# Optimization experiments

Measured on AMD Instinct MI355X. Metric: run time of the kernel, lower is better.

## Reference

```python
import jax, jax.numpy as jnp
import numpy as np

N_NODES = 50000
N_EDGES = 800000
FEAT = 10
HID = 64
N_SHEETS = 256
SHEET_LEN = 128
NUM_GRAPHS = 1


def _glorot(key, shape):
    fan_in, fan_out = shape[0], shape[1]
    lim = float(np.sqrt(6.0 / (fan_in + fan_out)))
    return jax.random.uniform(key, shape, jnp.float32, -lim, lim)


def setup_inputs() -> dict:
    key = jax.random.key(0)
    ks = jax.random.split(key, 16)
    x = jax.random.normal(ks[0], (N_NODES, FEAT), jnp.float32)
    edge_index = jax.random.randint(ks[1], (2, N_EDGES), 0, N_NODES, jnp.int64)
    batch = jnp.zeros((N_NODES,), jnp.int64)
    sheet_node_idx = jax.random.randint(ks[2], (N_SHEETS, SHEET_LEN), 0, N_NODES, jnp.int64)
    sheet_features = jax.random.normal(ks[3], (N_SHEETS, FEAT), jnp.float32)
    return {
        "x": x, "edge_index": edge_index, "batch": batch,
        "sheet_node_idx": sheet_node_idx, "sheet_features": sheet_features,
        "W_gcn1": _glorot(ks[4], (FEAT, HID)), "b_gcn1": jnp.zeros((HID,), jnp.float32),
        "W_gcn2": _glorot(ks[5], (HID, HID)), "b_gcn2": jnp.zeros((HID,), jnp.float32),
        "W_gcn3": _glorot(ks[6], (HID, HID)), "b_gcn3": jnp.zeros((HID,), jnp.float32),
        "geo_W1": _glorot(ks[7], (FEAT, HID)), "geo_b1": jnp.zeros((HID,), jnp.float32),
        "geo_W2": _glorot(ks[8], (HID, HID)), "geo_b2": jnp.zeros((HID,), jnp.float32),
        "fus_W": _glorot(ks[9], (2 * HID, HID)), "fus_b": jnp.zeros((HID,), jnp.float32),
        "q_W1": _glorot(ks[10], (2 * HID, HID)), "q_b1": jnp.zeros((HID,), jnp.float32),
        "q_W2": _glorot(ks[11], (HID, 1)), "q_b2": jnp.zeros((1,), jnp.float32),
    }


def gcn_conv(x, W, b, src, dst, norm_edge, norm_self):
    # PyG GCNConv: h = x @ W, symmetric-normalized aggregation with self loops, + b
    h = x @ W                                  # [N, H]
    msg = h[src] * norm_edge[:, None]          # [E, H] gather
    agg = jax.ops.segment_sum(msg, dst, num_segments=x.shape[0])  # scatter-add
    agg = agg + h * norm_self[:, None]         # self-loop contribution
    return agg + b


def reference(x, edge_index, batch, sheet_node_idx, sheet_features,
              W_gcn1, b_gcn1, W_gcn2, b_gcn2, W_gcn3, b_gcn3,
              geo_W1, geo_b1, geo_W2, geo_b2, fus_W, fus_b,
              q_W1, q_b1, q_W2, q_b2):
    src, dst = edge_index[0], edge_index[1]
    N = x.shape[0]
    # degree with self loops (edge weights = 1), counted on destination
    deg = jax.ops.segment_sum(jnp.ones_like(dst, jnp.float32), dst, num_segments=N) + 1.0
    dinv = jax.lax.rsqrt(deg)
    norm_edge = dinv[src] * dinv[dst]   # [E]
    norm_self = dinv * dinv             # [N]

    h = jax.nn.relu(gcn_conv(x, W_gcn1, b_gcn1, src, dst, norm_edge, norm_self))
    h = jax.nn.relu(gcn_conv(h, W_gcn2, b_gcn2, src, dst, norm_edge, norm_self))
    h = jax.nn.relu(gcn_conv(h, W_gcn3, b_gcn3, src, dst, norm_edge, norm_self))

    # global mean pool over batch ids (single graph here)
    sums = jax.ops.segment_sum(h, batch, num_segments=NUM_GRAPHS)
    counts = jax.ops.segment_sum(jnp.ones((N,), jnp.float32), batch, num_segments=NUM_GRAPHS)
    g_emb = sums / counts[:, None]      # [1, H]

    # per-sheet mean pooling (equal-length sheets)
    sheet_embs = h[sheet_node_idx].mean(axis=1)            # [S, H]

    geo = jax.nn.relu(sheet_features @ geo_W1 + geo_b1) @ geo_W2 + geo_b2
    fused = jax.nn.relu(jnp.concatenate([sheet_embs, geo], axis=1) @ fus_W + fus_b)

    global_embs = jnp.broadcast_to(g_emb, (fused.shape[0], g_emb.shape[1]))
    hq = jnp.concatenate([fused, global_embs], axis=1)
    q = jax.nn.relu(hq @ q_W1 + q_b1) @ q_W2 + q_b2
    return q[:, 0]
```

## Files before the change

### kernel.cpp

```cpp
#include <hip/hip_runtime.h>

#define HID 64
#define FEAT 10
#define MAXSEG 8192

typedef unsigned short u16;

__device__ inline u16 f2bf(float f) {
    unsigned u = __float_as_uint(f);
    unsigned r = (u + 0x7fffu + ((u >> 16) & 1u)) >> 16;
    return (u16)r;
}
__device__ inline void bf8_add(float* acc, uint4 u) {
    acc[0] += __uint_as_float(u.x << 16);
    acc[1] += __uint_as_float(u.x & 0xffff0000u);
    acc[2] += __uint_as_float(u.y << 16);
    acc[3] += __uint_as_float(u.y & 0xffff0000u);
    acc[4] += __uint_as_float(u.z << 16);
    acc[5] += __uint_as_float(u.z & 0xffff0000u);
    acc[6] += __uint_as_float(u.w << 16);
    acc[7] += __uint_as_float(u.w & 0xffff0000u);
}


__global__ void histA(const int* __restrict__ dst, int* __restrict__ cnt2T,
                      int E, int nbuckets, int nchunks) {
    __shared__ int lh[256];
    int t = threadIdx.x, c = blockIdx.x;
    if (t < 256) lh[t] = 0;
    __syncthreads();
    int base = c * 4096;
    #pragma unroll
    for (int j = 0; j < 4; j++) {
        int e = base + t + j * 1024;
        if (e < E) atomicAdd(&lh[dst[e] >> 8], 1);
    }
    __syncthreads();
    if (t < nbuckets) cnt2T[t * nchunks + c] = lh[t];
}

__global__ void off2_local(const int* __restrict__ cnt2T, int* __restrict__ off2L,
                           int* __restrict__ tot, int nchunks) {
    __shared__ int lds[256];
    int b = blockIdx.x, t = threadIdx.x;
    int v = (t < nchunks) ? cnt2T[b * nchunks + t] : 0;
    lds[t] = v;
    __syncthreads();
    for (int off = 1; off < 256; off <<= 1) {
        int a = lds[t];
        int s = (t >= off) ? lds[t - off] : 0;
        __syncthreads();
        lds[t] = a + s;
        __syncthreads();
    }
    if (t < nchunks) off2L[b * nchunks + t] = lds[t] - v;
    if (t == 255) tot[b] = lds[255];
}

__global__ void base_scan(const int* __restrict__ tot, int* __restrict__ base, int nbuckets) {
    __shared__ int lds[256];
    int t = threadIdx.x;
    int v = (t < nbuckets) ? tot[t] : 0;
    lds[t] = v;
    __syncthreads();
    for (int off = 1; off < 256; off <<= 1) {
        int a = lds[t];
        int s = (t >= off) ? lds[t - off] : 0;
        __syncthreads();
        lds[t] = a + s;
        __syncthreads();
    }
    if (t < nbuckets) base[t] = lds[t] - v;
}

__global__ void binpass(const int* __restrict__ src, const int* __restrict__ dst,
                        const int* __restrict__ base, const int* __restrict__ off2L,
                        unsigned* __restrict__ tmp, int E, int nbuckets, int nchunks) {
    __shared__ int cur[256];
    int t = threadIdx.x, c = blockIdx.x;
    if (t < 256) cur[t] = (t < nbuckets) ? base[t] + off2L[t * nchunks + c] : 0;
    __syncthreads();
    int b0 = c * 4096;
    #pragma unroll
    for (int j = 0; j < 4; j++) {
        int e = b0 + t + j * 1024;
        if (e < E) {
            int s = src[e], d = dst[e];
            int slot = atomicAdd(&cur[d >> 8], 1);
            tmp[slot] = ((unsigned)(d & 255) << 16) | (unsigned)s;
        }
    }
}

__global__ void csr_build(const unsigned* __restrict__ tmp, const int* __restrict__ base,
                          const int* __restrict__ tot, u16* __restrict__ csr2,
                          int* __restrict__ row_start, int* __restrict__ row_cntp,
                          float* __restrict__ dinv, int N) {
    __shared__ __align__(16) u16 staged[MAXSEG];
    __shared__ int cntL[256], padL[256], scanL[256], curL[256];
    int b = blockIdx.x, t = threadIdx.x;
    if (t < 256) cntL[t] = 0;
    for (int i = t; i < MAXSEG; i += 1024) staged[i] = (u16)N;
    __syncthreads();
    int segBase = base[b], segLen = tot[b];
    for (int i = t; i < segLen; i += 1024)
        atomicAdd(&cntL[tmp[segBase + i] >> 16], 1);
    __syncthreads();
    if (t < 256) { padL[t] = (cntL[t] + 7) & ~7; scanL[t] = padL[t]; }
    __syncthreads();
    for (int off = 1; off < 256; off <<= 1) {
        int a = (t < 256) ? scanL[t] : 0;
        int s = (t >= off && t < 256) ? scanL[t - off] : 0;
        __syncthreads();
        if (t < 256) scanL[t] = a + s;
        __syncthreads();
    }
    if (t < 256) {
        int excl = scanL[t] - padL[t];
        curL[t] = excl;
        int node = b * 256 + t;
        if (node < N) {
            row_start[node] = b * MAXSEG + excl;
            row_cntp[node]  = padL[t];
            dinv[node]      = rsqrtf((float)cntL[t] + 1.0f);
        }
    }
    __syncthreads();
    for (int i = t; i < segLen; i += 1024) {
        unsigned e = tmp[segBase + i];
        int idx = atomicAdd(&curL[e >> 16], 1);
        staged[idx] = (u16)(e & 0xffffu);
    }
    __syncthreads();
    ((uint4*)(csr2 + (size_t)b * MAXSEG))[t] = ((const uint4*)staged)[t];
}

__global__ void zero_sentinel(u16* __restrict__ hwb, u16* __restrict__ xp, int N) {
    int t = threadIdx.x;
    if (t < 64) hwb[((size_t)(t >> 4) * (N + 1) + N) * 16 + (t & 15)] = 0;
    else if (t < 80) xp[(size_t)N * 16 + (t - 64)] = 0;
}


__global__ void pad_x(const float* __restrict__ x, const float* __restrict__ dinv,
                      u16* __restrict__ xp, int N) {
    int idx = blockIdx.x * 256 + threadIdx.x;
    if (idx >= N * 16) return;
    int n = idx >> 4, c = idx & 15;
    xp[idx] = (c < FEAT) ? f2bf(dinv[n] * x[n * FEAT + c]) : (u16)0;
}

__global__ void gather_x(const int* __restrict__ row_start, const int* __restrict__ row_cntp,
                         const u16* __restrict__ csr2, const u16* __restrict__ xp,
                         const float* __restrict__ dinv, float* __restrict__ aggx, int N) {
    int t = threadIdx.x;
    int node = blockIdx.x * 128 + (t >> 1);
    if (node >= N) return;
    int c0 = (t & 1) * 8;
    float acc[8] = {0.f,0.f,0.f,0.f,0.f,0.f,0.f,0.f};
    uint4 sv = *(const uint4*)(xp + (size_t)node * 16 + c0);
    bf8_add(acc, sv);
    int i0 = row_start[node], iE = i0 + row_cntp[node];
    for (int i = i0; i < iE; i += 8) {
        uint4 ev = *(const uint4*)(csr2 + i);
        int s0 = ev.x & 0xffff, s1 = ev.x >> 16;
        int s2 = ev.y & 0xffff, s3 = ev.y >> 16;
        int s4 = ev.z & 0xffff, s5 = ev.z >> 16;
        int s6 = ev.w & 0xffff, s7 = ev.w >> 16;
        uint4 u0 = *(const uint4*)(xp + (size_t)s0 * 16 + c0);
        uint4 u1 = *(const uint4*)(xp + (size_t)s1 * 16 + c0);
        uint4 u2 = *(const uint4*)(xp + (size_t)s2 * 16 + c0);
        uint4 u3 = *(const uint4*)(xp + (size_t)s3 * 16 + c0);
        uint4 u4 = *(const uint4*)(xp + (size_t)s4 * 16 + c0);
        uint4 u5 = *(const uint4*)(xp + (size_t)s5 * 16 + c0);
        uint4 u6 = *(const uint4*)(xp + (size_t)s6 * 16 + c0);
        uint4 u7 = *(const uint4*)(xp + (size_t)s7 * 16 + c0);
        bf8_add(acc, u0); bf8_add(acc, u1); bf8_add(acc, u2); bf8_add(acc, u3);
        bf8_add(acc, u4); bf8_add(acc, u5); bf8_add(acc, u6); bf8_add(acc, u7);
    }
    float di = dinv[node];
    float4 o0 = make_float4(acc[0]*di, acc[1]*di, acc[2]*di, acc[3]*di);
    float4 o1 = make_float4(acc[4]*di, acc[5]*di, acc[6]*di, acc[7]*di);
    *(float4*)(aggx + (size_t)node * 16 + c0)     = o0;
    *(float4*)(aggx + (size_t)node * 16 + c0 + 4) = o1;
}

__global__ void gcn_matmul1(const float* __restrict__ aggx, const float* __restrict__ W1,
                            const float* __restrict__ b1, float* __restrict__ h1, int N) {
    __shared__ float sW[FEAT * 64];
    __shared__ float sH[64 * 16];
    int t = threadIdx.x;
    int node0 = blockIdx.x * 64;
    for (int i = t; i < FEAT * 64; i += 256) sW[i] = W1[i];
    for (int i = t; i < 64 * 16; i += 256) {
        int r = i >> 4, k = i & 15;
        int node = node0 + r;
        sH[i] = (node < N) ? aggx[(size_t)node * 16 + k] : 0.0f;
    }
    __syncthreads();
    int c0 = (t & 15) * 4;
    int rbase = (t >> 4) * 4;
    float4 a0 = {0,0,0,0}, a1 = {0,0,0,0}, a2 = {0,0,0,0}, a3 = {0,0,0,0};
    for (int k = 0; k < FEAT; k++) {
        float4 w = *(const float4*)(sW + k * 64 + c0);
        float h0 = sH[(rbase + 0) * 16 + k];
        float h1v = sH[(rbase + 1) * 16 + k];
        float h2 = sH[(rbase + 2) * 16 + k];
        float h3 = sH[(rbase + 3) * 16 + k];
        a0.x += h0 * w.x; a0.y += h0 * w.y; a0.z += h0 * w.z; a0.w += h0 * w.w;
        a1.x += h1v * w.x; a1.y += h1v * w.y; a1.z += h1v * w.z; a1.w += h1v * w.w;
        a2.x += h2 * w.x; a2.y += h2 * w.y; a2.z += h2 * w.z; a2.w += h2 * w.w;
        a3.x += h3 * w.x; a3.y += h3 * w.y; a3.z += h3 * w.z; a3.w += h3 * w.w;
    }
    float4 bb = *(const float4*)(b1 + c0);
    float4 accs[4] = {a0, a1, a2, a3};
    for (int rr = 0; rr < 4; rr++) {
        int node = node0 + rbase + rr;
        if (node >= N) break;
        float4 v = accs[rr];
        v.x = fmaxf(v.x + bb.x, 0.f); v.y = fmaxf(v.y + bb.y, 0.f);
        v.z = fmaxf(v.z + bb.z, 0.f); v.w = fmaxf(v.w + bb.w, 0.f);
        *(float4*)(h1 + (size_t)node * 64 + c0) = v;
    }
}


__global__ void gcn_matmul64(const float* __restrict__ h_in, const float* __restrict__ W,
                             const float* __restrict__ dinv, u16* __restrict__ hwb, int N) {
    __shared__ float sW[64 * 64];
    __shared__ float sH[64 * 65];
    int t = threadIdx.x;
    int node0 = blockIdx.x * 64;
    for (int i = t * 4; i < 4096; i += 1024)
        *(float4*)(sW + i) = *(const float4*)(W + i);
    for (int i = t; i < 4096; i += 256) {
        int r = i >> 6, k = i & 63;
        int node = node0 + r;
        sH[r * 65 + k] = (node < N) ? h_in[(size_t)node * 64 + k] : 0.0f;
    }
    __syncthreads();
    int c0 = (t & 15) * 4;
    int rbase = (t >> 4) * 4;
    float4 a0 = {0,0,0,0}, a1 = {0,0,0,0}, a2 = {0,0,0,0}, a3 = {0,0,0,0};
    for (int k = 0; k < 64; k++) {
        float4 w = *(const float4*)(sW + k * 64 + c0);
        float h0 = sH[(rbase + 0) * 65 + k];
        float h1v = sH[(rbase + 1) * 65 + k];
        float h2 = sH[(rbase + 2) * 65 + k];
        float h3 = sH[(rbase + 3) * 65 + k];
        a0.x += h0 * w.x; a0.y += h0 * w.y; a0.z += h0 * w.z; a0.w += h0 * w.w;
        a1.x += h1v * w.x; a1.y += h1v * w.y; a1.z += h1v * w.z; a1.w += h1v * w.w;
        a2.x += h2 * w.x; a2.y += h2 * w.y; a2.z += h2 * w.z; a2.w += h2 * w.w;
        a3.x += h3 * w.x; a3.y += h3 * w.y; a3.z += h3 * w.z; a3.w += h3 * w.w;
    }
    int slice = c0 >> 4;
    int cin   = c0 & 15;
    float4 accs[4] = {a0, a1, a2, a3};
    for (int rr = 0; rr < 4; rr++) {
        int node = node0 + rbase + rr;
        if (node >= N) break;
        float di = dinv[node];
        float4 v = accs[rr];
        ushort4 o;
        o.x = f2bf(v.x * di); o.y = f2bf(v.y * di);
        o.z = f2bf(v.z * di); o.w = f2bf(v.w * di);
        *(ushort4*)(hwb + ((size_t)slice * (N + 1) + node) * 16 + cin) = o;
    }
}

__global__ void gather_bf(const int* __restrict__ row_start, const int* __restrict__ row_cntp,
                          const u16* __restrict__ csr2, const u16* __restrict__ hwb,
                          const float* __restrict__ dinv, const float* __restrict__ b,
                          float* __restrict__ out, float* __restrict__ gsum,
                          int N, int do_gsum) {
    int t = threadIdx.x;
    int slice = blockIdx.x & 3;
    int nodeBlk = blockIdx.x >> 2;
    int nl = t >> 1;
    int node = nodeBlk * 128 + nl;
    int q = t & 1;
    int c0 = q * 8;
    const u16* hb = hwb + (size_t)slice * (N + 1) * 16;
    float acc[8] = {0.f,0.f,0.f,0.f,0.f,0.f,0.f,0.f};
    if (node < N) {
        uint4 sv = *(const uint4*)(hb + (size_t)node * 16 + c0);
        bf8_add(acc, sv);
        int i0 = row_start[node], iE = i0 + row_cntp[node];
        for (int i = i0; i < iE; i += 8) {
            uint4 ev = *(const uint4*)(csr2 + i);
            int s0 = ev.x & 0xffff, s1 = ev.x >> 16;
            int s2 = ev.y & 0xffff, s3 = ev.y >> 16;
            int s4 = ev.z & 0xffff, s5 = ev.z >> 16;
            int s6 = ev.w & 0xffff, s7 = ev.w >> 16;
            uint4 u0 = *(const uint4*)(hb + (size_t)s0 * 16 + c0);
            uint4 u1 = *(const uint4*)(hb + (size_t)s1 * 16 + c0);
            uint4 u2 = *(const uint4*)(hb + (size_t)s2 * 16 + c0);
            uint4 u3 = *(const uint4*)(hb + (size_t)s3 * 16 + c0);
            uint4 u4 = *(const uint4*)(hb + (size_t)s4 * 16 + c0);
            uint4 u5 = *(const uint4*)(hb + (size_t)s5 * 16 + c0);
            uint4 u6 = *(const uint4*)(hb + (size_t)s6 * 16 + c0);
            uint4 u7 = *(const uint4*)(hb + (size_t)s7 * 16 + c0);
            bf8_add(acc, u0); bf8_add(acc, u1); bf8_add(acc, u2); bf8_add(acc, u3);
            bf8_add(acc, u4); bf8_add(acc, u5); bf8_add(acc, u6); bf8_add(acc, u7);
        }
        float di = dinv[node];
        int cg = slice * 16 + c0;
        const float4 bb0 = *(const float4*)(b + cg);
        const float4 bb1 = *(const float4*)(b + cg + 4);
        float4 o0, o1;
        o0.x = fmaxf(acc[0]*di + bb0.x, 0.f); o0.y = fmaxf(acc[1]*di + bb0.y, 0.f);
        o0.z = fmaxf(acc[2]*di + bb0.z, 0.f); o0.w = fmaxf(acc[3]*di + bb0.w, 0.f);
        o1.x = fmaxf(acc[4]*di + bb1.x, 0.f); o1.y = fmaxf(acc[5]*di + bb1.y, 0.f);
        o1.z = fmaxf(acc[6]*di + bb1.z, 0.f); o1.w = fmaxf(acc[7]*di + bb1.w, 0.f);
        *(float4*)(out + (size_t)node * 64 + cg)     = o0;
        *(float4*)(out + (size_t)node * 64 + cg + 4) = o1;
        acc[0]=o0.x; acc[1]=o0.y; acc[2]=o0.z; acc[3]=o0.w;
        acc[4]=o1.x; acc[5]=o1.y; acc[6]=o1.z; acc[7]=o1.w;
    } else {
        for (int j = 0; j < 8; j++) acc[j] = 0.f;
    }
    if (do_gsum) {
        __shared__ float red[128 * 16];
        for (int j = 0; j < 8; j++) red[nl * 16 + c0 + j] = acc[j];
        __syncthreads();
        if (t < 16) {
            float s = 0.f;
            for (int k = 0; k < 128; k++) s += red[k * 16 + t];
            atomicAdd(&gsum[slice * 16 + t], s);
        }
    }
}


__global__ void final_kernel(const float* __restrict__ h3, const int* __restrict__ sheet_idx,
                             const float* __restrict__ sheet_feat, const float* __restrict__ g_sum,
                             const float* __restrict__ gW1, const float* __restrict__ gb1,
                             const float* __restrict__ gW2, const float* __restrict__ gb2,
                             const float* __restrict__ fW,  const float* __restrict__ fb,
                             const float* __restrict__ qW1, const float* __restrict__ qb1,
                             const float* __restrict__ qW2, const float* __restrict__ qb2,
                             float* __restrict__ out, int N, int L) {
    int s = blockIdx.x, t = threadIdx.x;
    __shared__ float red[256];
    __shared__ float semb[64];
    __shared__ float geoh[64];
    __shared__ float geo[64];
    __shared__ float hq[128];
    int c = t & 63, jg = t >> 6;
    float acc = 0.0f;
    for (int j = jg; j < L; j += 4) {
        int node = sheet_idx[s * L + j];
        acc += h3[(size_t)node * 64 + c];
    }
    red[t] = acc;
    __syncthreads();
    if (t < 64) {
        semb[t] = (red[t] + red[t + 64] + red[t + 128] + red[t + 192]) / (float)L;
        hq[64 + t] = g_sum[t] / (float)N;
        float a = gb1[t];
        #pragma unroll
        for (int k = 0; k < FEAT; k++) a += sheet_feat[s * FEAT + k] * gW1[k * 64 + t];
        geoh[t] = fmaxf(a, 0.0f);
    }
    __syncthreads();
    if (t < 64) {
        float a = gb2[t];
        for (int k = 0; k < 64; k++) a += geoh[k] * gW2[k * 64 + t];
        geo[t] = a;
    }
    __syncthreads();
    if (t < 64) {
        float a = fb[t];
        for (int k = 0; k < 64; k++) a += semb[k] * fW[k * 64 + t];
        for (int k = 0; k < 64; k++) a += geo[k]  * fW[(64 + k) * 64 + t];
        hq[t] = fmaxf(a, 0.0f);
    }
    __syncthreads();
    float q = 0.0f;
    if (t < 64) {
        float a = qb1[t];
        for (int k = 0; k < 128; k++) a += hq[k] * qW1[k * 64 + t];
        a = fmaxf(a, 0.0f);
        q = a * qW2[t];
        for (int off = 32; off > 0; off >>= 1) q += __shfl_down(q, off, 64);
        if (t == 0) out[s] = q + qb2[0];
    }
}

extern "C" void kernel_launch(void* const* d_in, const int* in_sizes, int n_in,
                              void* d_out, int out_size, void* d_ws, size_t ws_size,
                              hipStream_t stream) {
    const float* x          = (const float*)d_in[0];
    const int*   edge       = (const int*)d_in[1];
    const int*   sheet_idx  = (const int*)d_in[3];
    const float* sheet_feat = (const float*)d_in[4];
    const float* W1 = (const float*)d_in[5];  const float* b1 = (const float*)d_in[6];
    const float* W2 = (const float*)d_in[7];  const float* b2 = (const float*)d_in[8];
    const float* W3 = (const float*)d_in[9];  const float* b3 = (const float*)d_in[10];
    const float* gW1 = (const float*)d_in[11]; const float* gb1 = (const float*)d_in[12];
    const float* gW2 = (const float*)d_in[13]; const float* gb2 = (const float*)d_in[14];
    const float* fW  = (const float*)d_in[15]; const float* fb  = (const float*)d_in[16];
    const float* qW1 = (const float*)d_in[17]; const float* qb1 = (const float*)d_in[18];
    const float* qW2 = (const float*)d_in[19]; const float* qb2 = (const float*)d_in[20];
    float* out = (float*)d_out;

    int N = in_sizes[2];
    int E = in_sizes[1] / 2;
    int S = in_sizes[4] / FEAT;
    int L = in_sizes[3] / S;

    int nbuckets = (N + 255) / 256;
    int nchunks  = (E + 4095) / 4096;

    char* p = (char*)d_ws;
    unsigned* tmp  = (unsigned*)p;             p += (size_t)E * 4;
    u16* csr2      = (u16*)p;                  p += (size_t)nbuckets * MAXSEG * 2;
    float* hf      = (float*)p;                p += (size_t)N * 64 * 4;
    u16* hwb       = (u16*)p;                  p += (size_t)4 * (N + 1) * 16 * 2;
    u16* xp        = (u16*)p;                  p += (size_t)(N + 1) * 16 * 2;
    float* aggx    = (float*)p;                p += (size_t)N * 16 * 4;
    int* row_start = (int*)p;                  p += (size_t)N * 4;
    int* row_cntp  = (int*)p;                  p += (size_t)N * 4;
    float* dinv    = (float*)p;                p += (size_t)N * 4;
    float* gsum    = (float*)p;                p += 64 * 4;
    int* cnt2T     = (int*)p;                  p += (size_t)nbuckets * nchunks * 4;
    int* off2L     = (int*)p;                  p += (size_t)nbuckets * nchunks * 4;
    int* tot       = (int*)p;                  p += 256 * 4;
    int* base      = (int*)p;

    hipMemsetAsync(gsum, 0, 64 * 4, stream);

    const int* src = edge;
    const int* dst = edge + E;

    int gMM = (N + 63) / 64;
    int nodeBlocks = (N + 127) / 128;
    int gGB = 4 * nodeBlocks;
    int gPX = (N * 16 + 255) / 256;

    histA<<<nchunks, 1024, 0, stream>>>(dst, cnt2T, E, nbuckets, nchunks);
    off2_local<<<nbuckets, 256, 0, stream>>>(cnt2T, off2L, tot, nchunks);
    base_scan<<<1, 256, 0, stream>>>(tot, base, nbuckets);
    binpass<<<nchunks, 1024, 0, stream>>>(src, dst, base, off2L, tmp, E, nbuckets, nchunks);
    csr_build<<<nbuckets, 1024, 0, stream>>>(tmp, base, tot, csr2, row_start, row_cntp, dinv, N);
    zero_sentinel<<<1, 128, 0, stream>>>(hwb, xp, N);

    pad_x<<<gPX, 256, 0, stream>>>(x, dinv, xp, N);
    gather_x<<<nodeBlocks, 256, 0, stream>>>(row_start, row_cntp, csr2, xp, dinv, aggx, N);
    gcn_matmul1<<<gMM, 256, 0, stream>>>(aggx, W1, b1, hf, N);

    gcn_matmul64<<<gMM, 256, 0, stream>>>(hf, W2, dinv, hwb, N);
    gather_bf<<<gGB, 256, 0, stream>>>(row_start, row_cntp, csr2, hwb, dinv, b2, hf, gsum, N, 0);

    gcn_matmul64<<<gMM, 256, 0, stream>>>(hf, W3, dinv, hwb, N);
    gather_bf<<<gGB, 256, 0, stream>>>(row_start, row_cntp, csr2, hwb, dinv, b3, hf, gsum, N, 1);

    final_kernel<<<S, 256, 0, stream>>>(hf, sheet_idx, sheet_feat, gsum,
                                        gW1, gb1, gW2, gb2, fW, fb,
                                        qW1, qb1, qW2, qb2, out, N, L);
}
```

Baseline: 241.9 us.

## Sort nodes by padded degree class to balance warp work in gathers

Adds a counting sort (histogram, offset scan, base, scatter) that builds a permutation of nodes grouped by padded in-degree class, and the gather kernels process nodes in that order so lanes in a wavefront have similar loop trip counts. Row start and count are also packed into one int2 to save a load. This is meant to cut divergence from uneven degrees, at the cost of four extra small kernel launches and scattered output writes and source reads for permuted nodes.

Measured after the change: 251.6 us. 1.04x slower.

```diff
diff --git a/kernel.cpp b/kernel.cpp
--- a/kernel.cpp
+++ b/kernel.cpp
@@ -94,8 +94,7 @@
 
 __global__ void csr_build(const unsigned* __restrict__ tmp, const int* __restrict__ base,
                           const int* __restrict__ tot, u16* __restrict__ csr2,
-                          int* __restrict__ row_start, int* __restrict__ row_cntp,
-                          float* __restrict__ dinv, int N) {
+                          int2* __restrict__ rowinfo, float* __restrict__ dinv, int N) {
     __shared__ __align__(16) u16 staged[MAXSEG];
     __shared__ int cntL[256], padL[256], scanL[256], curL[256];
     int b = blockIdx.x, t = threadIdx.x;
@@ -120,9 +119,8 @@
         curL[t] = excl;
         int node = b * 256 + t;
         if (node < N) {
-            row_start[node] = b * MAXSEG + excl;
-            row_cntp[node]  = padL[t];
-            dinv[node]      = rsqrtf((float)cntL[t] + 1.0f);
+            rowinfo[node] = make_int2(b * MAXSEG + excl, padL[t]);
+            dinv[node]    = rsqrtf((float)cntL[t] + 1.0f);
         }
     }
     __syncthreads();
@@ -139,6 +137,58 @@
     int t = threadIdx.x;
     if (t < 64) hwb[((size_t)(t >> 4) * (N + 1) + N) * 16 + (t & 15)] = 0;
     else if (t < 80) xp[(size_t)N * 16 + (t - 64)] = 0;
+}
+
+
+__global__ void class_hist(const int2* __restrict__ rowinfo, int* __restrict__ cls2T,
+                           int N, int nchunkN) {
+    __shared__ int lh[16];
+    int t = threadIdx.x, c = blockIdx.x;
+    if (t < 16) lh[t] = 0;
+    __syncthreads();
+    int node = c * 256 + t;
+    if (node < N) atomicAdd(&lh[min(rowinfo[node].y >> 3, 15)], 1);
+    __syncthreads();
+    if (t < 16) cls2T[t * nchunkN + c] = lh[t];
+}
+
+__global__ void class_off(const int* __restrict__ cls2T, int* __restrict__ clsOffL,
+                          int* __restrict__ clsTot, int nchunkN) {
+    __shared__ int lds[256];
+    int b = blockIdx.x, t = threadIdx.x;
+    int v = (t < nchunkN) ? cls2T[b * nchunkN + t] : 0;
+    lds[t] = v;
+    __syncthreads();
+    for (int off = 1; off < 256; off <<= 1) {
+        int a = lds[t];
+        int s = (t >= off) ? lds[t - off] : 0;
+        __syncthreads();
+        lds[t] = a + s;
+        __syncthreads();
+    }
+    if (t < nchunkN) clsOffL[b * nchunkN + t] = lds[t] - v;
+    if (t == 255) clsTot[b] = lds[255];
+}
+
+__global__ void class_base(const int* __restrict__ clsTot, int* __restrict__ clsBase) {
+    if (threadIdx.x == 0) {
+        int run = 0;
+        for (int i = 0; i < 16; i++) { clsBase[i] = run; run += clsTot[i]; }
+    }
+}
+
+__global__ void perm_scatter(const int2* __restrict__ rowinfo, const int* __restrict__ clsBase,
+                             const int* __restrict__ clsOffL, int* __restrict__ perm,
+                             int N, int nchunkN) {
+    __shared__ int cur[16];
+    int t = threadIdx.x, c = blockIdx.x;
+    if (t < 16) cur[t] = clsBase[t] + clsOffL[t * nchunkN + c];
+    __syncthreads();
+    int node = c * 256 + t;
+    if (node < N) {
+        int pos = atomicAdd(&cur[min(rowinfo[node].y >> 3, 15)], 1);
+        perm[pos] = node;
+    }
 }
 
 
@@ -150,17 +200,19 @@
     xp[idx] = (c < FEAT) ? f2bf(dinv[n] * x[n * FEAT + c]) : (u16)0;
 }
 
-__global__ void gather_x(const int* __restrict__ row_start, const int* __restrict__ row_cntp,
+__global__ void gather_x(const int* __restrict__ perm, const int2* __restrict__ rowinfo,
                          const u16* __restrict__ csr2, const u16* __restrict__ xp,
                          const float* __restrict__ dinv, float* __restrict__ aggx, int N) {
     int t = threadIdx.x;
-    int node = blockIdx.x * 128 + (t >> 1);
-    if (node >= N) return;
+    int gid = blockIdx.x * 128 + (t >> 1);
+    if (gid >= N) return;
+    int node = perm[gid];
     int c0 = (t & 1) * 8;
     float acc[8] = {0.f,0.f,0.f,0.f,0.f,0.f,0.f,0.f};
     uint4 sv = *(const uint4*)(xp + (size_t)node * 16 + c0);
     bf8_add(acc, sv);
-    int i0 = row_start[node], iE = i0 + row_cntp[node];
+    int2 ri = rowinfo[node];
+    int i0 = ri.x, iE = ri.x + ri.y;
     for (int i = i0; i < iE; i += 8) {
         uint4 ev = *(const uint4*)(csr2 + i);
         int s0 = ev.x & 0xffff, s1 = ev.x >> 16;
@@ -268,7 +320,7 @@
     }
 }
 
-__global__ void gather_bf(const int* __restrict__ row_start, const int* __restrict__ row_cntp,
+__global__ void gather_bf(const int* __restrict__ perm, const int2* __restrict__ rowinfo,
                           const u16* __restrict__ csr2, const u16* __restrict__ hwb,
                           const float* __restrict__ dinv, const float* __restrict__ b,
                           float* __restrict__ out, float* __restrict__ gsum,
@@ -277,15 +329,17 @@
     int slice = blockIdx.x & 3;
     int nodeBlk = blockIdx.x >> 2;
     int nl = t >> 1;
-    int node = nodeBlk * 128 + nl;
+    int gid = nodeBlk * 128 + nl;
     int q = t & 1;
     int c0 = q * 8;
     const u16* hb = hwb + (size_t)slice * (N + 1) * 16;
     float acc[8] = {0.f,0.f,0.f,0.f,0.f,0.f,0.f,0.f};
-    if (node < N) {
+    if (gid < N) {
+        int node = perm[gid];
         uint4 sv = *(const uint4*)(hb + (size_t)node * 16 + c0);
         bf8_add(acc, sv);
-        int i0 = row_start[node], iE = i0 + row_cntp[node];
+        int2 ri = rowinfo[node];
+        int i0 = ri.x, iE = ri.x + ri.y;
         for (int i = i0; i < iE; i += 8) {
             uint4 ev = *(const uint4*)(csr2 + i);
             int s0 = ev.x & 0xffff, s1 = ev.x >> 16;
@@ -411,6 +465,7 @@
 
     int nbuckets = (N + 255) / 256;
     int nchunks  = (E + 4095) / 4096;
+    int nchunkN  = (N + 255) / 256;
 
     char* p = (char*)d_ws;
     unsigned* tmp  = (unsigned*)p;             p += (size_t)E * 4;
@@ -419,14 +474,18 @@
     u16* hwb       = (u16*)p;                  p += (size_t)4 * (N + 1) * 16 * 2;
     u16* xp        = (u16*)p;                  p += (size_t)(N + 1) * 16 * 2;
     float* aggx    = (float*)p;                p += (size_t)N * 16 * 4;
-    int* row_start = (int*)p;                  p += (size_t)N * 4;
-    int* row_cntp  = (int*)p;                  p += (size_t)N * 4;
+    int2* rowinfo  = (int2*)p;                 p += (size_t)N * 8;
+    int* perm      = (int*)p;                  p += (size_t)N * 4;
     float* dinv    = (float*)p;                p += (size_t)N * 4;
     float* gsum    = (float*)p;                p += 64 * 4;
     int* cnt2T     = (int*)p;                  p += (size_t)nbuckets * nchunks * 4;
     int* off2L     = (int*)p;                  p += (size_t)nbuckets * nchunks * 4;
     int* tot       = (int*)p;                  p += 256 * 4;
-    int* base      = (int*)p;
+    int* base      = (int*)p;                  p += 256 * 4;
+    int* cls2T     = (int*)p;                  p += (size_t)16 * nchunkN * 4;
+    int* clsOffL   = (int*)p;                  p += (size_t)16 * nchunkN * 4;
+    int* clsTot    = (int*)p;                  p += 16 * 4;
+    int* clsBase   = (int*)p;
 
     hipMemsetAsync(gsum, 0, 64 * 4, stream);
 
@@ -442,18 +501,23 @@
     off2_local<<<nbuckets, 256, 0, stream>>>(cnt2T, off2L, tot, nchunks);
     base_scan<<<1, 256, 0, stream>>>(tot, base, nbuckets);
     binpass<<<nchunks, 1024, 0, stream>>>(src, dst, base, off2L, tmp, E, nbuckets, nchunks);
-    csr_build<<<nbuckets, 1024, 0, stream>>>(tmp, base, tot, csr2, row_start, row_cntp, dinv, N);
+    csr_build<<<nbuckets, 1024, 0, stream>>>(tmp, base, tot, csr2, rowinfo, dinv, N);
     zero_sentinel<<<1, 128, 0, stream>>>(hwb, xp, N);
 
+    class_hist<<<nchunkN, 256, 0, stream>>>(rowinfo, cls2T, N, nchunkN);
+    class_off<<<16, 256, 0, stream>>>(cls2T, clsOffL, clsTot, nchunkN);
+    class_base<<<1, 64, 0, stream>>>(clsTot, clsBase);
+    perm_scatter<<<nchunkN, 256, 0, stream>>>(rowinfo, clsBase, clsOffL, perm, N, nchunkN);
+
     pad_x<<<gPX, 256, 0, stream>>>(x, dinv, xp, N);
-    gather_x<<<nodeBlocks, 256, 0, stream>>>(row_start, row_cntp, csr2, xp, dinv, aggx, N);
+    gather_x<<<nodeBlocks, 256, 0, stream>>>(perm, rowinfo, csr2, xp, dinv, aggx, N);
     gcn_matmul1<<<gMM, 256, 0, stream>>>(aggx, W1, b1, hf, N);
 
     gcn_matmul64<<<gMM, 256, 0, stream>>>(hf, W2, dinv, hwb, N);
-    gather_bf<<<gGB, 256, 0, stream>>>(row_start, row_cntp, csr2, hwb, dinv, b2, hf, gsum, N, 0);
+    gather_bf<<<gGB, 256, 0, stream>>>(perm, rowinfo, csr2, hwb, dinv, b2, hf, gsum, N, 0);
 
     gcn_matmul64<<<gMM, 256, 0, stream>>>(hf, W3, dinv, hwb, N);
-    gather_bf<<<gGB, 256, 0, stream>>>(row_start, row_cntp, csr2, hwb, dinv, b3, hf, gsum, N, 1);
+    gather_bf<<<gGB, 256, 0, stream>>>(perm, rowinfo, csr2, hwb, dinv, b3, hf, gsum, N, 1);
 
     final_kernel<<<S, 256, 0, stream>>>(hf, sheet_idx, sheet_feat, gsum,
                                         gW1, gb1, gW2, gb2, fW, fb,
```
